# Kernel tuning notes

Measured on AMD Instinct MI355X. Metric: run time of the kernel, lower is better.

Reference implementation:

```python
import jax, jax.numpy as jnp
import numpy as np

NEG_SLOPE = 0.01  # torch LeakyReLU default

def setup_inputs() -> dict:
    key = jax.random.key(0)
    ks = jax.random.split(key, 8)
    B, T, D = 8, 2048, 512
    E, H = 8, 2 * D  # n_experts, ffn hidden
    s = 0.02
    return {
        "x":  jax.random.normal(ks[0], (B, T, D), dtype=jnp.float32),
        "Wr": jax.random.normal(ks[1], (D, E), dtype=jnp.float32) * s,
        "br": jnp.zeros((E,), dtype=jnp.float32),
        "W1": jax.random.normal(ks[2], (E, D, H), dtype=jnp.float32) * s,
        "b1": jnp.zeros((E, H), dtype=jnp.float32),
        "W2": jax.random.normal(ks[3], (E, H, D), dtype=jnp.float32) * s,
        "b2": jnp.zeros((E, D), dtype=jnp.float32),
    }

def reference(x, Wr, br, W1, b1, W2, b2):
    B, T, D = x.shape
    E = Wr.shape[1]
    top_k = 2
    balancing_coef = 1e-4
    x_flat = x.reshape(B * T, D)  # [N, D]

    # router: softmax over experts
    router_probs = jax.nn.softmax(x_flat @ Wr + br, axis=-1)  # [N, E]
    top_weights, top_indices = jax.lax.top_k(router_probs, top_k)  # [N, k]

    # dense all-expert FFN (faithful to original: every expert on every token)
    h = jax.nn.leaky_relu(jnp.einsum('nd,edh->neh', x_flat, W1) + b1, NEG_SLOPE)  # [N, E, H]
    expert_out = jax.nn.leaky_relu(jnp.einsum('neh,ehd->ned', h, W2) + b2, NEG_SLOPE)  # [N, E, D]
    # dropout is identity in eval mode

    # gather top-k expert outputs and combine with router weights
    top_out = jnp.take_along_axis(expert_out, top_indices[:, :, None], axis=1)  # [N, k, D]
    out_flat = jnp.sum(top_out * top_weights[:, :, None], axis=1)  # [N, D]
    output = out_flat.reshape(B, T, D)

    # load-balancing loss
    target = jnp.full((E,), 1.0 / E, dtype=x.dtype)
    mean_probs = jnp.mean(router_probs, axis=0)
    gating_loss = jnp.mean((target - mean_probs) ** 2) * balancing_coef
    return (output, gating_loss)
```

## Files before the change

### kernel.cpp

```cpp
#include <hip/hip_runtime.h>
#include <hip/hip_bf16.h>

constexpr int D_    = 512;
constexpr int H_    = 1024;
constexpr int E_    = 8;
constexpr int NTOK_ = 16384;
constexpr int MT_   = 64;
constexpr float NEG_ = 0.01f;

typedef short s16x8 __attribute__((ext_vector_type(8)));
typedef float f32x4 __attribute__((ext_vector_type(4)));

#define MFMA16(a,b,c) __builtin_amdgcn_mfma_f32_16x16x32_bf16((a),(b),(c),0,0,0)

__device__ __forceinline__ unsigned short f2bf(float f) {
  unsigned u = __float_as_uint(f);
  u += 0x7FFFu + ((u >> 16) & 1u);
  return (unsigned short)(u >> 16);
}
__device__ __forceinline__ float bf2f(unsigned u16) {
  return __uint_as_float(u16 << 16);
}
__device__ __forceinline__ float leaky(float v) {
  return v > 0.f ? v : NEG_ * v;
}

__global__ __launch_bounds__(256) void prep_kernel(
    const float* __restrict__ x, const float* __restrict__ Wr,
    const float* __restrict__ br,
    const float* __restrict__ W1, const float* __restrict__ W2,
    unsigned short* __restrict__ W1s, unsigned short* __restrict__ W2s,
    unsigned short* __restrict__ xbf1, unsigned short* __restrict__ xbf2,
    int* __restrict__ cnt, float* __restrict__ psum,
    int* __restrict__ tokE, int* __restrict__ tokSlot, float* __restrict__ tokW,
    int* __restrict__ tokOfPosE) {
  const int blk = blockIdx.x;
  const int tid = threadIdx.x;
  __shared__ float SH[8256 + 32];
  if (blk < 256) {
    const int t0 = blk * 64;
    unsigned short* xbf = (t0 < 8192) ? xbf1 + (size_t)t0 * D_
                                      : xbf2 + (size_t)(t0 - 8192) * D_;
    float* xt   = SH;
    float* red  = SH;
    float* lp   = SH + 8256;
    int*  lcnt  = (int*)(SH + 8256 + 8);
    int*  gbase = (int*)(SH + 8256 + 16);
    if (tid < 8) { lcnt[tid] = 0; lp[tid] = 0.f; }

    const int tq = tid & 63;
    const int q  = tid >> 6;
    float acc[E_];
#pragma unroll
    for (int e = 0; e < E_; e++) acc[e] = 0.f;

    for (int c = 0; c < 4; c++) {
      __syncthreads();
#pragma unroll
      for (int it = 0; it < 8; it++) {
        int f = it * 256 + tid;
        int row = f >> 5, c4 = f & 31;
        float4 v = *(const float4*)(x + (size_t)(t0 + row) * D_ + c * 128 + c4 * 4);
        float* d = xt + row * 129 + c4 * 4;
        d[0] = v.x; d[1] = v.y; d[2] = v.z; d[3] = v.w;
        ushort4 pk;
        pk.x = f2bf(v.x); pk.y = f2bf(v.y);
        pk.z = f2bf(v.z); pk.w = f2bf(v.w);
        *(ushort4*)(xbf + (size_t)row * D_ + c * 128 + c4 * 4) = pk;
      }
      __syncthreads();
#pragma unroll
      for (int j = 0; j < 32; j++) {
        float xv = xt[tq * 129 + q * 32 + j];
        const float* wr = Wr + (size_t)(c * 128 + q * 32 + j) * E_;
#pragma unroll
        for (int e = 0; e < E_; e++) acc[e] += xv * wr[e];
      }
    }
    __syncthreads();
#pragma unroll
    for (int e = 0; e < E_; e++) red[(q * 64 + tq) * 8 + e] = acc[e];
    __syncthreads();

    float m1 = -1.f, m2 = -1.f; int i1 = 0, i2 = 0, s1 = 0, s2 = 0;
    if (tid < 64) {
      float p[E_];
#pragma unroll
      for (int e = 0; e < E_; e++)
        p[e] = br[e] + red[tid * 8 + e] + red[(64 + tid) * 8 + e]
             + red[(128 + tid) * 8 + e] + red[(192 + tid) * 8 + e];
      float mx = p[0];
#pragma unroll
      for (int e = 1; e < E_; e++) mx = fmaxf(mx, p[e]);
      float s = 0.f;
#pragma unroll
      for (int e = 0; e < E_; e++) { p[e] = expf(p[e] - mx); s += p[e]; }
      float inv = 1.f / s;
#pragma unroll
      for (int e = 0; e < E_; e++) p[e] *= inv;

#pragma unroll
      for (int e = 0; e < E_; e++) {
        float pe = p[e];
        if (pe > m1)      { m2 = m1; i2 = i1; m1 = pe; i1 = e; }
        else if (pe > m2) { m2 = pe; i2 = e; }
      }
      s1 = atomicAdd(&lcnt[i1], 1);
      s2 = atomicAdd(&lcnt[i2], 1);
#pragma unroll
      for (int e = 0; e < E_; e++) atomicAdd(&lp[e], p[e]);
    }
    __syncthreads();
    if (tid < 8) {
      gbase[tid] = atomicAdd(&cnt[tid * 16], lcnt[tid]);
      atomicAdd(&psum[tid * 16], lp[tid]);
    }
    __syncthreads();
    if (tid < 64) {
      int gt = t0 + tid;
      int sl1 = gbase[i1] + s1, sl2 = gbase[i2] + s2;
      tokE[2 * gt]     = i1; tokSlot[2 * gt]     = sl1; tokW[2 * gt]     = m1;
      tokE[2 * gt + 1] = i2; tokSlot[2 * gt + 1] = sl2; tokW[2 * gt + 1] = m2;
      tokOfPosE[i1 * NTOK_ + sl1] = gt;
      tokOfPosE[i2 * NTOK_ + sl2] = gt;
    }
  } else {
    float* ldsf = SH;
    int bid = blk - 256;
    const float* src;
    int eE, kt, tc, srcStride;
    bool isW1 = bid < 1024;
    if (isW1) {
      eE = bid >> 7; kt = (bid >> 4) & 7; tc = bid & 15; srcStride = 1024;
      src = W1 + ((size_t)(eE * 512 + kt * 64)) * 1024 + tc * 64;
    } else {
      int b2i = bid - 1024;
      eE = b2i >> 7; kt = (b2i >> 3) & 15; tc = b2i & 7; srcStride = 512;
      src = W2 + ((size_t)(eE * 1024 + kt * 64)) * 512 + tc * 64;
    }
#pragma unroll
    for (int rep = 0; rep < 4; rep++) {
      int row = rep * 16 + (tid >> 4);
      int c4  = (tid & 15) * 4;
      float4 v = *(const float4*)(src + (size_t)row * srcStride + c4);
      float* d = ldsf + row * 68 + c4;
      d[0] = v.x; d[1] = v.y; d[2] = v.z; d[3] = v.w;
    }
    __syncthreads();
    int wv = tid >> 6, lane = tid & 63;
#pragma unroll
    for (int qi = 0; qi < 2; qi++) {
      int qq = wv * 2 + qi;
      int ks = qq >> 2, nt = qq & 3;
      int k0 = ks * 32 + (lane >> 4) * 8;
      int n  = nt * 16 + (lane & 15);
      s16x8 v;
#pragma unroll
      for (int j = 0; j < 8; j++) v[j] = (short)f2bf(ldsf[(k0 + j) * 68 + n]);
      int ntg = tc * 4 + nt, kkg = kt * 2 + ks;
      if (isW1)
        *(s16x8*)(W1s + (((size_t)eE << 16) + (ntg << 10) + (kkg << 6) + lane) * 8) = v;
      else
        *(s16x8*)(W2s + (((size_t)eE << 16) + (ntg << 11) + (kkg << 6) + lane) * 8) = v;
    }
  }
}

__global__ __launch_bounds__(512, 2) void ffn_kernel(
    const unsigned short* __restrict__ xbf1, const unsigned short* __restrict__ xbf2,
    const unsigned short* __restrict__ W1s, const unsigned short* __restrict__ W2s,
    const float* __restrict__ b1, const float* __restrict__ b2,
    const int* __restrict__ cnt, const int* __restrict__ tokOfPosE,
    unsigned short* __restrict__ buf) {
  const int e = blockIdx.x & 7;
  const int tile = blockIdx.x >> 3;
  int nTok = 0, base0 = 0;
#pragma unroll
  for (int i = 0; i < E_; i++) {
    int ci = cnt[i * 16];
    if (i < e) base0 += ci;
    if (i == e) nTok = ci;
  }
  const int start = tile * MT_;
  if (start >= nTok) return;
  const int valid = min(MT_, nTok - start);
  const int base = base0 + start;

  __shared__ __align__(16) unsigned short L[MT_][1032];

  const int tid = threadIdx.x;
  const int w = tid >> 6;
  const int lane = tid & 63;

  for (int r = w; r < MT_; r += 8) {
    int tok = tokOfPosE[e * NTOK_ + start + min(r, valid - 1)];
    const unsigned short* srow = (tok < 8192)
        ? xbf1 + (size_t)tok * D_
        : xbf2 + (size_t)(tok - 8192) * D_;
    s16x8 v = *(const s16x8*)(srow + lane * 8);
    *(s16x8*)&L[r][lane * 8] = v;
  }
  __syncthreads();

  const int qm = lane & 15;
  const int qk = (lane >> 4) * 8;
  const int qr = (lane >> 4) * 4;

  const unsigned short* A1 =
      W1s + (((size_t)e << 16) + ((size_t)(w * 8) << 10) + lane) * 8;
  f32x4 acc1[8][4];
#pragma unroll
  for (int mi = 0; mi < 8; mi++)
#pragma unroll
    for (int ni = 0; ni < 4; ni++) acc1[mi][ni] = {0.f, 0.f, 0.f, 0.f};

  s16x8 a1p[2][8];
#pragma unroll
  for (int s = 0; s < 2; s++)
#pragma unroll
    for (int mi = 0; mi < 8; mi++)
      a1p[s][mi] = *(const s16x8*)(A1 + (size_t)mi * 8192 + s * 512);

#pragma unroll
  for (int kk = 0; kk < 16; kk++) {
    s16x8 bcur[4];
#pragma unroll
    for (int ni = 0; ni < 4; ni++)
      bcur[ni] = *(const s16x8*)&L[ni * 16 + qm][kk * 32 + qk];
    __builtin_amdgcn_s_setprio(1);
#pragma unroll
    for (int mi = 0; mi < 8; mi++)
#pragma unroll
      for (int ni = 0; ni < 4; ni++)
        acc1[mi][ni] = MFMA16(a1p[kk & 1][mi], bcur[ni], acc1[mi][ni]);
    __builtin_amdgcn_s_setprio(0);
    if (kk + 2 < 16) {
#pragma unroll
      for (int mi = 0; mi < 8; mi++)
        a1p[kk & 1][mi] = *(const s16x8*)(A1 + (size_t)mi * 8192 + (kk + 2) * 512);
    }
  }
  __syncthreads();

  const unsigned short* A2 =
      W2s + (((size_t)e << 16) + ((size_t)(w * 4) << 11) + lane) * 8;
  s16x8 a2p[2][4];
#pragma unroll
  for (int s = 0; s < 2; s++)
#pragma unroll
    for (int mi = 0; mi < 4; mi++)
      a2p[s][mi] = *(const s16x8*)(A2 + (size_t)mi * 16384 + s * 512);

#pragma unroll
  for (int mi = 0; mi < 8; mi++) {
    int hb = w * 128 + mi * 16 + qr;
    float4 bv = *(const float4*)(b1 + (size_t)e * H_ + hb);
#pragma unroll
    for (int ni = 0; ni < 4; ni++) {
      int tr = ni * 16 + qm;
      ushort4 pk;
      pk.x = f2bf(leaky(acc1[mi][ni][0] + bv.x));
      pk.y = f2bf(leaky(acc1[mi][ni][1] + bv.y));
      pk.z = f2bf(leaky(acc1[mi][ni][2] + bv.z));
      pk.w = f2bf(leaky(acc1[mi][ni][3] + bv.w));
      *(ushort4*)&L[tr][hb] = pk;
    }
  }
  __syncthreads();

  f32x4 acc2[4][4];
#pragma unroll
  for (int mi = 0; mi < 4; mi++)
#pragma unroll
    for (int ni = 0; ni < 4; ni++) acc2[mi][ni] = {0.f, 0.f, 0.f, 0.f};

#pragma unroll
  for (int kk = 0; kk < 32; kk++) {
    s16x8 bcur[4];
#pragma unroll
    for (int ni = 0; ni < 4; ni++)
      bcur[ni] = *(const s16x8*)&L[ni * 16 + qm][kk * 32 + qk];
    __builtin_amdgcn_s_setprio(1);
#pragma unroll
    for (int mi = 0; mi < 4; mi++)
#pragma unroll
      for (int ni = 0; ni < 4; ni++)
        acc2[mi][ni] = MFMA16(a2p[kk & 1][mi], bcur[ni], acc2[mi][ni]);
    __builtin_amdgcn_s_setprio(0);
    if (kk + 2 < 32) {
#pragma unroll
      for (int mi = 0; mi < 4; mi++)
        a2p[kk & 1][mi] = *(const s16x8*)(A2 + (size_t)mi * 16384 + (kk + 2) * 512);
    }
  }

#pragma unroll
  for (int mi = 0; mi < 4; mi++) {
    int ob = w * 64 + mi * 16 + qr;
    float4 bv = *(const float4*)(b2 + (size_t)e * D_ + ob);
#pragma unroll
    for (int ni = 0; ni < 4; ni++) {
      int tok = ni * 16 + qm;
      if (tok < valid) {
        ushort4 pk;
        pk.x = f2bf(leaky(acc2[mi][ni][0] + bv.x));
        pk.y = f2bf(leaky(acc2[mi][ni][1] + bv.y));
        pk.z = f2bf(leaky(acc2[mi][ni][2] + bv.z));
        pk.w = f2bf(leaky(acc2[mi][ni][3] + bv.w));
        *(ushort4*)(buf + (size_t)(base + tok) * D_ + ob) = pk;
      }
    }
  }
}

__global__ __launch_bounds__(256) void combine_kernel(
    const unsigned short* __restrict__ buf,
    const int* __restrict__ tokE, const int* __restrict__ tokSlot,
    const float* __restrict__ tokW,
    const int* __restrict__ cnt, const float* __restrict__ psum,
    float* __restrict__ out, float* __restrict__ loss_out) {
  __shared__ int soff[E_];
  if (threadIdx.x == 0) {
    int o = 0;
#pragma unroll
    for (int e = 0; e < E_; e++) { soff[e] = o; o += cnt[e * 16]; }
  }
  __syncthreads();
  if (blockIdx.x == 0 && threadIdx.x == 0) {
    float l = 0.f;
#pragma unroll
    for (int e = 0; e < E_; e++) {
      float d = 0.125f - psum[e * 16] / (float)NTOK_;
      l += d * d;
    }
    *loss_out = (l / 8.f) * 1e-4f;
  }
  int t = blockIdx.x * 4 + (threadIdx.x >> 6);
  int lane = threadIdx.x & 63;
  int p0 = soff[tokE[2 * t]]     + tokSlot[2 * t];
  int p1 = soff[tokE[2 * t + 1]] + tokSlot[2 * t + 1];
  float w0 = tokW[2 * t], w1 = tokW[2 * t + 1];
  uint4 u0 = ((const uint4*)(buf + (size_t)p0 * D_))[lane];
  uint4 u1 = ((const uint4*)(buf + (size_t)p1 * D_))[lane];
  float4 oA, oB;
  oA.x = w0 * bf2f(u0.x & 0xFFFFu) + w1 * bf2f(u1.x & 0xFFFFu);
  oA.y = w0 * bf2f(u0.x >> 16)     + w1 * bf2f(u1.x >> 16);
  oA.z = w0 * bf2f(u0.y & 0xFFFFu) + w1 * bf2f(u1.y & 0xFFFFu);
  oA.w = w0 * bf2f(u0.y >> 16)     + w1 * bf2f(u1.y >> 16);
  oB.x = w0 * bf2f(u0.z & 0xFFFFu) + w1 * bf2f(u1.z & 0xFFFFu);
  oB.y = w0 * bf2f(u0.z >> 16)     + w1 * bf2f(u1.z >> 16);
  oB.z = w0 * bf2f(u0.w & 0xFFFFu) + w1 * bf2f(u1.w & 0xFFFFu);
  oB.w = w0 * bf2f(u0.w >> 16)     + w1 * bf2f(u1.w >> 16);
  float4* dst = (float4*)(out + (size_t)t * D_);
  dst[lane * 2]     = oA;
  dst[lane * 2 + 1] = oB;
}

extern "C" void kernel_launch(void* const* d_in, const int* in_sizes, int n_in,
                              void* d_out, int out_size, void* d_ws, size_t ws_size,
                              hipStream_t stream) {
  const float* x  = (const float*)d_in[0];
  const float* Wr = (const float*)d_in[1];
  const float* br = (const float*)d_in[2];
  const float* W1 = (const float*)d_in[3];
  const float* b1 = (const float*)d_in[4];
  const float* W2 = (const float*)d_in[5];
  const float* b2 = (const float*)d_in[6];
  float* out = (float*)d_out;

  char* ws = (char*)d_ws;
  int*   cnt      = (int*)(ws + 0);
  float* psum     = (float*)(ws + 512);
  int*   tokE     = (int*)(ws + 4096);
  int*   tokSlot  = (int*)(ws + 4096 + 1 * 131072);
  float* tokW     = (float*)(ws + 4096 + 2 * 131072);
  int*   tokOfPosE= (int*)(ws + 4096 + 3 * 131072);
  unsigned short* W1s  = (unsigned short*)(ws + (size_t)(1u << 20));
  unsigned short* xbf1 = (unsigned short*)(ws + (size_t)(1u << 20) + 8388608u);
  unsigned short* W2s  = (unsigned short*)(ws + (size_t)(1u << 20) + 16777216u);
  unsigned short* xbf2 = (unsigned short*)(ws + (size_t)(1u << 20) + 25165824u);
  unsigned short* buf  = (unsigned short*)(ws + (size_t)(1u << 20) + 33554432u);

  hipMemsetAsync(d_ws, 0, 2048, stream);
  prep_kernel<<<256 + 2048, 256, 0, stream>>>(x, Wr, br, W1, W2, W1s, W2s,
                                              xbf1, xbf2,
                                              cnt, psum, tokE, tokSlot, tokW,
                                              tokOfPosE);
  ffn_kernel<<<(NTOK_ / MT_) * E_, 512, 0, stream>>>(xbf1, xbf2, W1s, W2s,
                                                     b1, b2, cnt, tokOfPosE, buf);
  combine_kernel<<<NTOK_ / 4, 256, 0, stream>>>(buf, tokE, tokSlot, tokW,
                                                cnt, psum, out,
                                                out + (size_t)NTOK_ * D_);
}
```

Baseline: 256.2 us.

## Fuse top-k combine into FFN epilogue via weighted atomic adds

Removes the separate combine kernel and the bf16 intermediate buffer. The FFN epilogue now multiplies each expert output by its router weight and atomically adds it into the zeroed fp32 output, and it also computes the gating loss. A memset of the output is added. This trades a kernel launch plus a buffer write and read for many scalar float atomics, two per output element, and the summation order becomes nondeterministic.

```diff
diff --git a/kernel.cpp b/kernel.cpp
--- a/kernel.cpp
+++ b/kernel.cpp
@@ -32,8 +32,7 @@
     unsigned short* __restrict__ W1s, unsigned short* __restrict__ W2s,
     unsigned short* __restrict__ xbf1, unsigned short* __restrict__ xbf2,
     int* __restrict__ cnt, float* __restrict__ psum,
-    int* __restrict__ tokE, int* __restrict__ tokSlot, float* __restrict__ tokW,
-    int* __restrict__ tokOfPosE) {
+    int* __restrict__ tokOfPosE, float* __restrict__ wOfPosE) {
   const int blk = blockIdx.x;
   const int tid = threadIdx.x;
   __shared__ float SH[8256 + 32];
@@ -119,10 +118,10 @@
     if (tid < 64) {
       int gt = t0 + tid;
       int sl1 = gbase[i1] + s1, sl2 = gbase[i2] + s2;
-      tokE[2 * gt]     = i1; tokSlot[2 * gt]     = sl1; tokW[2 * gt]     = m1;
-      tokE[2 * gt + 1] = i2; tokSlot[2 * gt + 1] = sl2; tokW[2 * gt + 1] = m2;
       tokOfPosE[i1 * NTOK_ + sl1] = gt;
       tokOfPosE[i2 * NTOK_ + sl2] = gt;
+      wOfPosE[i1 * NTOK_ + sl1] = m1;
+      wOfPosE[i2 * NTOK_ + sl2] = m2;
     }
   } else {
     float* ldsf = SH;
@@ -170,8 +169,18 @@
     const unsigned short* __restrict__ xbf1, const unsigned short* __restrict__ xbf2,
     const unsigned short* __restrict__ W1s, const unsigned short* __restrict__ W2s,
     const float* __restrict__ b1, const float* __restrict__ b2,
-    const int* __restrict__ cnt, const int* __restrict__ tokOfPosE,
-    unsigned short* __restrict__ buf) {
+    const int* __restrict__ cnt, const float* __restrict__ psum,
+    const int* __restrict__ tokOfPosE, const float* __restrict__ wOfPosE,
+    float* __restrict__ out) {
+  if (blockIdx.x == 0 && threadIdx.x == 0) {
+    float l = 0.f;
+#pragma unroll
+    for (int i = 0; i < E_; i++) {
+      float d = 0.125f - psum[i * 16] / (float)NTOK_;
+      l += d * d;
+    }
+    out[(size_t)NTOK_ * D_] = (l / 8.f) * 1e-4f;
+  }
   const int e = blockIdx.x & 7;
   const int tile = blockIdx.x >> 3;
   int nTok = 0, base0 = 0;
@@ -184,7 +193,6 @@
   const int start = tile * MT_;
   if (start >= nTok) return;
   const int valid = min(MT_, nTok - start);
-  const int base = base0 + start;
 
   __shared__ __align__(16) unsigned short L[MT_][1032];
 
@@ -294,6 +302,14 @@
     }
   }
 
+  int tokv[4]; float wv[4];
+#pragma unroll
+  for (int ni = 0; ni < 4; ni++) {
+    int tok = ni * 16 + qm;
+    int idx = e * NTOK_ + start + min(tok, valid - 1);
+    tokv[ni] = tokOfPosE[idx];
+    wv[ni]   = wOfPosE[idx];
+  }
 #pragma unroll
   for (int mi = 0; mi < 4; mi++) {
     int ob = w * 64 + mi * 16 + qr;
@@ -302,58 +318,14 @@
     for (int ni = 0; ni < 4; ni++) {
       int tok = ni * 16 + qm;
       if (tok < valid) {
-        ushort4 pk;
-        pk.x = f2bf(leaky(acc2[mi][ni][0] + bv.x));
-        pk.y = f2bf(leaky(acc2[mi][ni][1] + bv.y));
-        pk.z = f2bf(leaky(acc2[mi][ni][2] + bv.z));
-        pk.w = f2bf(leaky(acc2[mi][ni][3] + bv.w));
-        *(ushort4*)(buf + (size_t)(base + tok) * D_ + ob) = pk;
+        float* dst = out + (size_t)tokv[ni] * D_ + ob;
+        atomicAdd(dst + 0, wv[ni] * leaky(acc2[mi][ni][0] + bv.x));
+        atomicAdd(dst + 1, wv[ni] * leaky(acc2[mi][ni][1] + bv.y));
+        atomicAdd(dst + 2, wv[ni] * leaky(acc2[mi][ni][2] + bv.z));
+        atomicAdd(dst + 3, wv[ni] * leaky(acc2[mi][ni][3] + bv.w));
       }
     }
   }
-}
-
-__global__ __launch_bounds__(256) void combine_kernel(
-    const unsigned short* __restrict__ buf,
-    const int* __restrict__ tokE, const int* __restrict__ tokSlot,
-    const float* __restrict__ tokW,
-    const int* __restrict__ cnt, const float* __restrict__ psum,
-    float* __restrict__ out, float* __restrict__ loss_out) {
-  __shared__ int soff[E_];
-  if (threadIdx.x == 0) {
-    int o = 0;
-#pragma unroll
-    for (int e = 0; e < E_; e++) { soff[e] = o; o += cnt[e * 16]; }
-  }
-  __syncthreads();
-  if (blockIdx.x == 0 && threadIdx.x == 0) {
-    float l = 0.f;
-#pragma unroll
-    for (int e = 0; e < E_; e++) {
-      float d = 0.125f - psum[e * 16] / (float)NTOK_;
-      l += d * d;
-    }
-    *loss_out = (l / 8.f) * 1e-4f;
-  }
-  int t = blockIdx.x * 4 + (threadIdx.x >> 6);
-  int lane = threadIdx.x & 63;
-  int p0 = soff[tokE[2 * t]]     + tokSlot[2 * t];
-  int p1 = soff[tokE[2 * t + 1]] + tokSlot[2 * t + 1];
-  float w0 = tokW[2 * t], w1 = tokW[2 * t + 1];
-  uint4 u0 = ((const uint4*)(buf + (size_t)p0 * D_))[lane];
-  uint4 u1 = ((const uint4*)(buf + (size_t)p1 * D_))[lane];
-  float4 oA, oB;
-  oA.x = w0 * bf2f(u0.x & 0xFFFFu) + w1 * bf2f(u1.x & 0xFFFFu);
-  oA.y = w0 * bf2f(u0.x >> 16)     + w1 * bf2f(u1.x >> 16);
-  oA.z = w0 * bf2f(u0.y & 0xFFFFu) + w1 * bf2f(u1.y & 0xFFFFu);
-  oA.w = w0 * bf2f(u0.y >> 16)     + w1 * bf2f(u1.y >> 16);
-  oB.x = w0 * bf2f(u0.z & 0xFFFFu) + w1 * bf2f(u1.z & 0xFFFFu);
-  oB.y = w0 * bf2f(u0.z >> 16)     + w1 * bf2f(u1.z >> 16);
-  oB.z = w0 * bf2f(u0.w & 0xFFFFu) + w1 * bf2f(u1.w & 0xFFFFu);
-  oB.w = w0 * bf2f(u0.w >> 16)     + w1 * bf2f(u1.w >> 16);
-  float4* dst = (float4*)(out + (size_t)t * D_);
-  dst[lane * 2]     = oA;
-  dst[lane * 2 + 1] = oB;
 }
 
 extern "C" void kernel_launch(void* const* d_in, const int* in_sizes, int n_in,
@@ -371,24 +343,19 @@
   char* ws = (char*)d_ws;
   int*   cnt      = (int*)(ws + 0);
   float* psum     = (float*)(ws + 512);
-  int*   tokE     = (int*)(ws + 4096);
-  int*   tokSlot  = (int*)(ws + 4096 + 1 * 131072);
-  float* tokW     = (float*)(ws + 4096 + 2 * 131072);
-  int*   tokOfPosE= (int*)(ws + 4096 + 3 * 131072);
+  int*   tokOfPosE= (int*)(ws + 4096);
   unsigned short* W1s  = (unsigned short*)(ws + (size_t)(1u << 20));
   unsigned short* xbf1 = (unsigned short*)(ws + (size_t)(1u << 20) + 8388608u);
   unsigned short* W2s  = (unsigned short*)(ws + (size_t)(1u << 20) + 16777216u);
   unsigned short* xbf2 = (unsigned short*)(ws + (size_t)(1u << 20) + 25165824u);
-  unsigned short* buf  = (unsigned short*)(ws + (size_t)(1u << 20) + 33554432u);
+  float* wOfPosE  = (float*)(ws + (size_t)(1u << 20) + 33554432u);
 
   hipMemsetAsync(d_ws, 0, 2048, stream);
+  hipMemsetAsync(d_out, 0, ((size_t)NTOK_ * D_ + 1) * sizeof(float), stream);
   prep_kernel<<<256 + 2048, 256, 0, stream>>>(x, Wr, br, W1, W2, W1s, W2s,
-                                              xbf1, xbf2,
-                                              cnt, psum, tokE, tokSlot, tokW,
-                                              tokOfPosE);
+                                              xbf1, xbf2, cnt, psum,
+                                              tokOfPosE, wOfPosE);
   ffn_kernel<<<(NTOK_ / MT_) * E_, 512, 0, stream>>>(xbf1, xbf2, W1s, W2s,
-                                                     b1, b2, cnt, tokOfPosE, buf);
-  combine_kernel<<<NTOK_ / 4, 256, 0, stream>>>(buf, tokE, tokSlot, tokW,
-                                                cnt, psum, out,
-                                                out + (size_t)NTOK_ * D_);
-}
+                                                     b1, b2, cnt, psum,
+                                                     tokOfPosE, wOfPosE, out);
+}
```

After: 424.3 us. +65.6%, slower.
